# Performance work log

Hardware: AMD Instinct MI355X
Metric: run time of the kernel (lower is better)

## Reference

```python
import jax, jax.numpy as jnp
import numpy as np

HEADS = 16

def setup_inputs() -> dict:
    key = jax.random.key(0)
    ks = jax.random.split(key, 5)
    B, T, D = 2, 2048, 2048
    s = 0.02
    return {
        "x": jax.random.normal(ks[0], (B, T, D), dtype=jnp.float32),
        "Wq": jax.random.normal(ks[1], (D, D), dtype=jnp.float32) * s,
        "Wk": jax.random.normal(ks[2], (D, D), dtype=jnp.float32) * s,
        "Wv": jax.random.normal(ks[3], (D, D), dtype=jnp.float32) * s,
        "Wo": jax.random.normal(ks[4], (D, D), dtype=jnp.float32) * s,
    }

def reference(x, Wq, Wk, Wv, Wo):
    B, T, _ = x.shape
    H = HEADS
    Dh = Wq.shape[1] // H
    # projections: [B,T,H,Dh]
    q = (x @ Wq).reshape(B, T, H, Dh)
    k = (x @ Wk).reshape(B, T, H, Dh)
    v = (x @ Wv).reshape(B, T, H, Dh)
    # raw scores [B,H,T,T]
    scores = jnp.einsum("bthd,bshd->bhts", q, k)
    # NOTE (faithful to source): mask is multiplicative 0/1 tril (the
    # masked_fill(-inf) in the torch code is not in-place and has no effect),
    # and the scale is sqrt(token_len), not sqrt(head_dim).
    mask = jnp.tril(jnp.ones((T, T), dtype=scores.dtype))
    scores = scores * mask
    attn = jax.nn.softmax(scores / (T ** 0.5), axis=-1)
    out = jnp.einsum("bhts,bshd->bthd", attn, v).reshape(B, T, H * Dh)
    return out @ Wo
```

## Files before the change

### kernel.cpp

```cpp
#include <hip/hip_runtime.h>


typedef __attribute__((ext_vector_type(4))) float  f32x4;
typedef __attribute__((ext_vector_type(8))) short  bf16x8;
typedef __attribute__((ext_vector_type(4))) unsigned short u16x4;

#define AS1 __attribute__((address_space(1)))
#define AS3 __attribute__((address_space(3)))

__device__ __forceinline__ void llds16(const void* g, void* l) {
  __builtin_amdgcn_global_load_lds((const AS1 void*)g, (AS3 void*)l, 16, 0, 0);
}

__device__ __forceinline__ unsigned short f2bf(float f) {
  unsigned int u = __builtin_bit_cast(unsigned int, f);
  u += 0x7fffu + ((u >> 16) & 1u);
  return (unsigned short)(u >> 16);
}

__device__ __forceinline__ float bf2f(unsigned short u) {
  return __builtin_bit_cast(float, (unsigned int)u << 16);
}

__global__ __launch_bounds__(256) void cast_x_kernel(const float* __restrict__ in,
                                                     unsigned short* __restrict__ out) {
  int i = blockIdx.x * 256 + threadIdx.x;
  f32x4 v = ((const f32x4*)in)[i];
  u16x4 o;
  o[0] = f2bf(v[0]); o[1] = f2bf(v[1]); o[2] = f2bf(v[2]); o[3] = f2bf(v[3]);
  ((u16x4*)out)[i] = o;
}

__global__ __launch_bounds__(256) void transpose_w_kernel(const float* __restrict__ W,
                                                          unsigned short* __restrict__ Wt) {
  __shared__ float tile[32][33];
  const int bx = blockIdx.x << 5;
  const int by = blockIdx.y << 5;
  const int tx = threadIdx.x;
  const int ty = threadIdx.y;
#pragma unroll
  for (int r = ty; r < 32; r += 8)
    tile[r][tx] = W[(size_t)(bx + r) * 2048 + by + tx];
  __syncthreads();
#pragma unroll
  for (int r = ty; r < 32; r += 8)
    Wt[(size_t)(by + r) * 2048 + bx + tx] = f2bf(tile[tx][r]);
}

template <int OUT>
__global__ __launch_bounds__(256) void gemm_bt(const unsigned short* __restrict__ A,
                                               const unsigned short* __restrict__ Bt,
                                               void* __restrict__ Cv) {
  __shared__ __align__(16) char smem[16384];
  const int tid  = threadIdx.x;
  const int lane = tid & 63;
  const int w    = tid >> 6;
  const int f    = blockIdx.x;
  const int bn   = ((f & 7) << 1) + ((f >> 3) & 1);
  const int bm   = f >> 4;
  const int wr = w >> 1, wc = w & 1;
  const int q16 = lane >> 4;
  const int l15 = lane & 15;

  f32x4 acc[4][4];
#pragma unroll
  for (int i = 0; i < 4; ++i)
#pragma unroll
    for (int j = 0; j < 4; ++j) acc[i][j] = (f32x4){0.f, 0.f, 0.f, 0.f};

  for (int k0 = 0; k0 < 2048; k0 += 32) {
    __syncthreads();
#pragma unroll
    for (int c = 0; c < 2; ++c) {
      int ch  = (w << 1) + c;
      int row = (ch << 4) + (lane >> 2);
      int colb = ((lane & 3) << 4) ^ (((row >> 1) & 3) << 4);
      const unsigned short* srcA = A + (size_t)((bm << 7) + row) * 2048 + k0 + (colb >> 1);
      llds16(srcA, smem + (ch << 10));
      const unsigned short* srcB = Bt + (size_t)((bn << 7) + row) * 2048 + k0 + (colb >> 1);
      llds16(srcB, smem + 8192 + (ch << 10));
    }
    asm volatile("s_waitcnt vmcnt(0)" ::: "memory");
    __syncthreads();

    bf16x8 af[4], bf[4];
#pragma unroll
    for (int mi = 0; mi < 4; ++mi) {
      int row = (wr << 6) + (mi << 4) + l15;
      af[mi] = *(const bf16x8*)(smem + (row << 6) + ((q16 << 4) ^ (((row >> 1) & 3) << 4)));
    }
#pragma unroll
    for (int ni = 0; ni < 4; ++ni) {
      int row = (wc << 6) + (ni << 4) + l15;
      bf[ni] = *(const bf16x8*)(smem + 8192 + (row << 6) + ((q16 << 4) ^ (((row >> 1) & 3) << 4)));
    }
#pragma unroll
    for (int mi = 0; mi < 4; ++mi)
#pragma unroll
      for (int ni = 0; ni < 4; ++ni)
        acc[mi][ni] = __builtin_amdgcn_mfma_f32_16x16x32_bf16(af[mi], bf[ni], acc[mi][ni], 0, 0, 0);
  }

  const int rb = q16 << 2;
#pragma unroll
  for (int mi = 0; mi < 4; ++mi) {
    int m0 = (bm << 7) + (wr << 6) + (mi << 4) + rb;
#pragma unroll
    for (int ni = 0; ni < 4; ++ni) {
      int n = (bn << 7) + (wc << 6) + (ni << 4) + l15;
      if constexpr (OUT == 0) {
        unsigned short* C = (unsigned short*)Cv;
#pragma unroll
        for (int j = 0; j < 4; ++j)
          C[(size_t)(m0 + j) * 2048 + n] = f2bf(acc[mi][ni][j]);
      } else if constexpr (OUT == 1) {
        u16x4 pk;
#pragma unroll
        for (int j = 0; j < 4; ++j) pk[j] = f2bf(acc[mi][ni][j]);
        int b = m0 >> 11, t = m0 & 2047;
        unsigned short* C = (unsigned short*)Cv;
        *(u16x4*)(C + ((size_t)((b << 4) + (n >> 7)) * 128 + (n & 127)) * 2048 + t) = pk;
      } else {
        float* C = (float*)Cv;
#pragma unroll
        for (int j = 0; j < 4; ++j)
          C[(size_t)(m0 + j) * 2048 + n] = acc[mi][ni][j];
      }
    }
  }
}

__global__ __launch_bounds__(256) void vsuf_kernel(const unsigned short* __restrict__ Vt,
                                                   float* __restrict__ Suf) {
  const int row  = blockIdx.x * 4 + (threadIdx.x >> 6);
  const int lane = threadIdx.x & 63;
  const unsigned short* vp = Vt + (size_t)row * 2048 + (lane << 5);
  float a = 0.f;
#pragma unroll
  for (int c = 0; c < 4; ++c) {
    bf16x8 v = *(const bf16x8*)(vp + (c << 3));
#pragma unroll
    for (int j = 0; j < 8; ++j) a += bf2f((unsigned short)v[j]);
  }
  float I = a;
#pragma unroll
  for (int off = 1; off < 64; off <<= 1) {
    float t = __shfl_down(I, off, 64);
    I += (lane + off < 64) ? t : 0.f;
  }
  Suf[(size_t)lane * 4096 + row] = I;
  if (lane == 0) Suf[(size_t)64 * 4096 + row] = 0.f;
}

__global__ __launch_bounds__(256) void attn_kernel(const unsigned short* __restrict__ Q,
                                                   const unsigned short* __restrict__ K,
                                                   const unsigned short* __restrict__ V,
                                                   const float* __restrict__ Suf,
                                                   unsigned short* __restrict__ O) {
  __shared__ __align__(16) char smem[36864];
  const int tid  = threadIdx.x;
  const int lane = tid & 63;
  const int w    = tid >> 6;
  const int q16  = lane >> 4;
  const int l15  = lane & 15;
  const int f    = blockIdx.x;
  const int bh    = ((f & 7) << 2) + ((f >> 3) & 3);
  const int strip = 31 - (f >> 5);
  const int b  = bh >> 4;
  const float scale = 0.02209708691207961f;
  const size_t qkbase = ((size_t)(b << 11)) * 2048 + ((size_t)(bh & 15) << 7);
  const size_t vbase  = (size_t)bh << 18;
  const int rb = q16 << 2;
  char* Psm = smem + 32768 + (w << 10);

  const int numIter = 2 * strip + 2;
  const int t0 = (strip << 6) + (w << 4);

  auto stage = [&](int s0, int kb, int vb) {
#pragma unroll
    for (int c = 0; c < 2; ++c) {
      int ch = (w << 1) + c;
      int rowK = (ch << 2) + q16;
      int colbK = (l15 << 4) ^ ((rowK & 7) << 4);
      llds16(K + qkbase + (size_t)(s0 + rowK) * 2048 + (colbK >> 1), smem + kb + (ch << 10));
      int rowV = (ch << 4) + (lane >> 2);
      int colbV = ((lane & 3) << 4) ^ (((rowV >> 2) & 3) << 4);
      llds16(V + vbase + (size_t)rowV * 2048 + s0 + (colbV >> 1), smem + vb + (ch << 10));
    }
  };

  bf16x8 qf[4];
  {
    const unsigned short* qp = Q + qkbase + (size_t)(t0 + l15) * 2048 + (q16 << 3);
#pragma unroll
    for (int kk = 0; kk < 4; ++kk) qf[kk] = *(const bf16x8*)(qp + (kk << 5));
  }

  f32x4 oacc[8];
#pragma unroll
  for (int i = 0; i < 8; ++i) oacc[i] = (f32x4){0.f, 0.f, 0.f, 0.f};
  float ell[4] = {0.f, 0.f, 0.f, 0.f};

  stage(0, 0, 16384);
  asm volatile("s_waitcnt vmcnt(0)" ::: "memory");
  __syncthreads();

  int cur = 0;
  for (int it = 0; it < numIter; ++it) {
    const int s0 = it << 5;
    if (it + 1 < numIter)
      stage(s0 + 32, (cur ^ 1) << 13, 16384 + ((cur ^ 1) << 13));

    if (s0 <= t0) {
      const int kb = cur << 13;
      const int vb = 16384 + (cur << 13);

      f32x4 sA = (f32x4){0.f, 0.f, 0.f, 0.f}, sB = (f32x4){0.f, 0.f, 0.f, 0.f};
#pragma unroll
      for (int kk = 0; kk < 4; ++kk) {
        int r0 = l15;
        bf16x8 k0f = *(const bf16x8*)(smem + kb + (r0 << 8) + (((kk << 6) + (q16 << 4)) ^ ((r0 & 7) << 4)));
        sA = __builtin_amdgcn_mfma_f32_16x16x32_bf16(qf[kk], k0f, sA, 0, 0, 0);
        int r1 = 16 + l15;
        bf16x8 k1f = *(const bf16x8*)(smem + kb + (r1 << 8) + (((kk << 6) + (q16 << 4)) ^ ((r1 & 7) << 4)));
        sB = __builtin_amdgcn_mfma_f32_16x16x32_bf16(qf[kk], k1f, sB, 0, 0, 0);
      }

      float pA[4], pB[4];
#pragma unroll
      for (int j = 0; j < 4; ++j) {
        int t  = t0 + rb + j;
        int sa = s0 + l15;
        float vA = (sa <= t)      ? sA[j] * scale : 0.f;
        float vB = (sa + 16 <= t) ? sB[j] * scale : 0.f;
        pA[j] = __expf(vA);
        pB[j] = __expf(vB);
        ell[j] += pA[j] + pB[j];
      }

#pragma unroll
      for (int j = 0; j < 4; ++j) {
        int r   = rb + j;
        int swz = ((r >> 1) & 3) << 4;
        *(unsigned short*)(Psm + (r << 6) + ((l15 << 1) ^ swz))        = f2bf(pA[j]);
        *(unsigned short*)(Psm + (r << 6) + ((32 + (l15 << 1)) ^ swz)) = f2bf(pB[j]);
      }
      asm volatile("s_waitcnt lgkmcnt(0)" ::: "memory");

      bf16x8 pa;
      {
        int r = l15;
        pa = *(const bf16x8*)(Psm + (r << 6) + ((q16 << 4) ^ (((r >> 1) & 3) << 4)));
      }
#pragma unroll
      for (int ni = 0; ni < 8; ++ni) {
        int dr = (ni << 4) + l15;
        bf16x8 vbf = *(const bf16x8*)(smem + vb + (dr << 6) + ((q16 << 4) ^ (((dr >> 2) & 3) << 4)));
        oacc[ni] = __builtin_amdgcn_mfma_f32_16x16x32_bf16(pa, vbf, oacc[ni], 0, 0, 0);
      }
    }

    asm volatile("s_waitcnt vmcnt(0)" ::: "memory");
    __syncthreads();
    cur ^= 1;
  }

  const int send = (t0 & ~31) + 32;
  const float* sp = Suf + (size_t)(send >> 5) * 4096 + ((size_t)bh << 7);
  const float extra = (float)(2048 - send);
#pragma unroll
  for (int ni = 0; ni < 8; ++ni) {
    float sv = sp[(ni << 4) + l15];
#pragma unroll
    for (int j = 0; j < 4; ++j) oacc[ni][j] += sv;
  }

#pragma unroll
  for (int j = 0; j < 4; ++j) {
    float r = ell[j];
    r += __shfl_xor(r, 1, 64);
    r += __shfl_xor(r, 2, 64);
    r += __shfl_xor(r, 4, 64);
    r += __shfl_xor(r, 8, 64);
    float inv = 1.0f / (r + extra);
    int t = t0 + rb + j;
    unsigned short* op = O + qkbase + (size_t)t * 2048;
#pragma unroll
    for (int ni = 0; ni < 8; ++ni)
      op[(ni << 4) + l15] = f2bf(oacc[ni][j] * inv);
  }
}

extern "C" void kernel_launch(void* const* d_in, const int* in_sizes, int n_in,
                              void* d_out, int out_size, void* d_ws, size_t ws_size,
                              hipStream_t stream) {
  (void)in_sizes; (void)n_in; (void)out_size; (void)ws_size;
  const float* x  = (const float*)d_in[0];
  const float* Wq = (const float*)d_in[1];
  const float* Wk = (const float*)d_in[2];
  const float* Wv = (const float*)d_in[3];
  const float* Wo = (const float*)d_in[4];
  float* out = (float*)d_out;

  char* ws = (char*)d_ws;
  unsigned short* Xb  = (unsigned short*)(ws);
  unsigned short* Wqt = (unsigned short*)(ws + 16777216);
  unsigned short* Wkt = (unsigned short*)(ws + 16777216 + 8388608);
  unsigned short* Wvt = (unsigned short*)(ws + 16777216 + 2 * 8388608);
  unsigned short* Wot = (unsigned short*)(ws + 16777216 + 3 * 8388608);
  unsigned short* Qb  = (unsigned short*)(ws + 50331648);
  unsigned short* Kb  = (unsigned short*)(ws + 67108864);
  unsigned short* Vt  = (unsigned short*)(ws + 83886080);
  unsigned short* Ob  = Xb;
  float*          Suf = (float*)Wqt;

  cast_x_kernel<<<8192, 256, 0, stream>>>(x, Xb);
  {
    dim3 tb(32, 8), tg(64, 64);
    transpose_w_kernel<<<tg, tb, 0, stream>>>(Wq, Wqt);
    transpose_w_kernel<<<tg, tb, 0, stream>>>(Wk, Wkt);
    transpose_w_kernel<<<tg, tb, 0, stream>>>(Wv, Wvt);
    transpose_w_kernel<<<tg, tb, 0, stream>>>(Wo, Wot);
  }
  gemm_bt<0><<<512, 256, 0, stream>>>(Xb, Wqt, (void*)Qb);
  gemm_bt<0><<<512, 256, 0, stream>>>(Xb, Wkt, (void*)Kb);
  gemm_bt<1><<<512, 256, 0, stream>>>(Xb, Wvt, (void*)Vt);

  vsuf_kernel<<<1024, 256, 0, stream>>>(Vt, Suf);

  attn_kernel<<<1024, 256, 0, stream>>>(Qb, Kb, Vt, Suf, Ob);

  gemm_bt<2><<<512, 256, 0, stream>>>(Ob, Wot, (void*)out);
}
```

Before: 305.8 us.

## Pipeline GEMM with 4-stage LDS buffering and 128x256 tiles per block

Reworks the bf16 GEMM so each 512-thread block computes a 128x256 tile and prefetches three K-steps ahead into a 4-slot LDS ring using global_load_lds. Counted vmcnt waits let global loads overlap MFMA compute. It also remaps block indices for XCD-aware locality and raises wave priority around the MFMAs. The cost is much more LDS per block (96KB), which limits occupancy, and the grid shrinks to 256 blocks, which may leave some CUs underused.

```diff
diff --git a/kernel.cpp b/kernel.cpp
--- a/kernel.cpp
+++ b/kernel.cpp
@@ -48,58 +48,97 @@
 }
 
 template <int OUT>
-__global__ __launch_bounds__(256) void gemm_bt(const unsigned short* __restrict__ A,
-                                               const unsigned short* __restrict__ Bt,
-                                               void* __restrict__ Cv) {
-  __shared__ __align__(16) char smem[16384];
+__global__ __launch_bounds__(512, 2) void gemm_bt(const unsigned short* __restrict__ A,
+                                                  const unsigned short* __restrict__ Bt,
+                                                  void* __restrict__ Cv) {
+  __shared__ __align__(16) char smem[98304];
   const int tid  = threadIdx.x;
   const int lane = tid & 63;
   const int w    = tid >> 6;
   const int f    = blockIdx.x;
-  const int bn   = ((f & 7) << 1) + ((f >> 3) & 1);
-  const int bm   = f >> 4;
-  const int wr = w >> 1, wc = w & 1;
+  const int xcd  = f & 7;
+  const int g    = f >> 3;
+  const int bm   = ((xcd >> 1) << 3) + (g & 7);
+  const int bn   = ((xcd & 1) << 2) + (g >> 3);
+  const int wr = w >> 2, wc = w & 3;
   const int q16 = lane >> 4;
   const int l15 = lane & 15;
 
+  const int aIdx = (w << 6) + lane;
+  const int aRow = aIdx >> 2, aCph = aIdx & 3;
+  const unsigned short* aSrc = A + (size_t)((bm << 7) + aRow) * 2048
+                                 + ((aCph ^ ((aRow >> 1) & 3)) << 3);
+  const int bRow0 = aIdx >> 2, bCph0 = aIdx & 3;
+  const int bIdx1 = 512 + aIdx;
+  const int bRow1 = bIdx1 >> 2, bCph1 = bIdx1 & 3;
+  const unsigned short* bSrc0 = Bt + (size_t)((bn << 8) + bRow0) * 2048
+                                  + ((bCph0 ^ ((bRow0 >> 1) & 3)) << 3);
+  const unsigned short* bSrc1 = Bt + (size_t)((bn << 8) + bRow1) * 2048
+                                  + ((bCph1 ^ ((bRow1 >> 1) & 3)) << 3);
+
+  const int swx = ((q16 ^ ((l15 >> 1) & 3)) << 4);
+  const int aoff = ((wr << 6) + l15) * 64 + swx;
+  const int boff = 8192 + ((wc << 6) + l15) * 64 + swx;
+
   f32x4 acc[4][4];
 #pragma unroll
   for (int i = 0; i < 4; ++i)
 #pragma unroll
     for (int j = 0; j < 4; ++j) acc[i][j] = (f32x4){0.f, 0.f, 0.f, 0.f};
 
-  for (int k0 = 0; k0 < 2048; k0 += 32) {
-    __syncthreads();
-#pragma unroll
-    for (int c = 0; c < 2; ++c) {
-      int ch  = (w << 1) + c;
-      int row = (ch << 4) + (lane >> 2);
-      int colb = ((lane & 3) << 4) ^ (((row >> 1) & 3) << 4);
-      const unsigned short* srcA = A + (size_t)((bm << 7) + row) * 2048 + k0 + (colb >> 1);
-      llds16(srcA, smem + (ch << 10));
-      const unsigned short* srcB = Bt + (size_t)((bn << 7) + row) * 2048 + k0 + (colb >> 1);
-      llds16(srcB, smem + 8192 + (ch << 10));
-    }
-    asm volatile("s_waitcnt vmcnt(0)" ::: "memory");
-    __syncthreads();
-
+  auto stageT = [&](int t, int slot) {
+    char* sb = smem + slot * 24576 + (w << 10);
+    const size_t ko = (size_t)t << 5;
+    llds16(aSrc + ko, sb);
+    llds16(bSrc0 + ko, sb + 8192);
+    llds16(bSrc1 + ko, sb + 16384);
+  };
+
+  auto computeT = [&](int slot) {
+    const char* base = smem + slot * 24576;
     bf16x8 af[4], bf[4];
 #pragma unroll
-    for (int mi = 0; mi < 4; ++mi) {
-      int row = (wr << 6) + (mi << 4) + l15;
-      af[mi] = *(const bf16x8*)(smem + (row << 6) + ((q16 << 4) ^ (((row >> 1) & 3) << 4)));
-    }
-#pragma unroll
-    for (int ni = 0; ni < 4; ++ni) {
-      int row = (wc << 6) + (ni << 4) + l15;
-      bf[ni] = *(const bf16x8*)(smem + 8192 + (row << 6) + ((q16 << 4) ^ (((row >> 1) & 3) << 4)));
-    }
+    for (int mi = 0; mi < 4; ++mi) af[mi] = *(const bf16x8*)(base + aoff + (mi << 10));
+#pragma unroll
+    for (int ni = 0; ni < 4; ++ni) bf[ni] = *(const bf16x8*)(base + boff + (ni << 10));
+    __builtin_amdgcn_s_setprio(1);
 #pragma unroll
     for (int mi = 0; mi < 4; ++mi)
 #pragma unroll
       for (int ni = 0; ni < 4; ++ni)
         acc[mi][ni] = __builtin_amdgcn_mfma_f32_16x16x32_bf16(af[mi], bf[ni], acc[mi][ni], 0, 0, 0);
-  }
+    __builtin_amdgcn_s_setprio(0);
+  };
+
+  stageT(0, 0); stageT(1, 1); stageT(2, 2);
+
+#pragma unroll 1
+  for (int i = 0; i < 60; i += 4) {
+#pragma unroll
+    for (int u = 0; u < 4; ++u) {
+      stageT(i + u + 3, (u + 3) & 3);
+      asm volatile("s_waitcnt vmcnt(9)" ::: "memory");
+      __builtin_amdgcn_s_barrier();
+      computeT(u);
+      __builtin_amdgcn_s_barrier();
+    }
+  }
+  stageT(63, 3);
+  asm volatile("s_waitcnt vmcnt(9)" ::: "memory");
+  __builtin_amdgcn_s_barrier();
+  computeT(0);
+  __builtin_amdgcn_s_barrier();
+  asm volatile("s_waitcnt vmcnt(6)" ::: "memory");
+  __builtin_amdgcn_s_barrier();
+  computeT(1);
+  __builtin_amdgcn_s_barrier();
+  asm volatile("s_waitcnt vmcnt(3)" ::: "memory");
+  __builtin_amdgcn_s_barrier();
+  computeT(2);
+  __builtin_amdgcn_s_barrier();
+  asm volatile("s_waitcnt vmcnt(0)" ::: "memory");
+  __builtin_amdgcn_s_barrier();
+  computeT(3);
 
   const int rb = q16 << 2;
 #pragma unroll
@@ -107,7 +146,7 @@
     int m0 = (bm << 7) + (wr << 6) + (mi << 4) + rb;
 #pragma unroll
     for (int ni = 0; ni < 4; ++ni) {
-      int n = (bn << 7) + (wc << 6) + (ni << 4) + l15;
+      int n = (bn << 8) + (wc << 6) + (ni << 4) + l15;
       if constexpr (OUT == 0) {
         unsigned short* C = (unsigned short*)Cv;
 #pragma unroll
@@ -322,13 +361,13 @@
     transpose_w_kernel<<<tg, tb, 0, stream>>>(Wv, Wvt);
     transpose_w_kernel<<<tg, tb, 0, stream>>>(Wo, Wot);
   }
-  gemm_bt<0><<<512, 256, 0, stream>>>(Xb, Wqt, (void*)Qb);
-  gemm_bt<0><<<512, 256, 0, stream>>>(Xb, Wkt, (void*)Kb);
-  gemm_bt<1><<<512, 256, 0, stream>>>(Xb, Wvt, (void*)Vt);
+  gemm_bt<0><<<256, 512, 0, stream>>>(Xb, Wqt, (void*)Qb);
+  gemm_bt<0><<<256, 512, 0, stream>>>(Xb, Wkt, (void*)Kb);
+  gemm_bt<1><<<256, 512, 0, stream>>>(Xb, Wvt, (void*)Vt);
 
   vsuf_kernel<<<1024, 256, 0, stream>>>(Vt, Suf);
 
   attn_kernel<<<1024, 256, 0, stream>>>(Qb, Kb, Vt, Suf, Ob);
 
-  gemm_bt<2><<<512, 256, 0, stream>>>(Ob, Wot, (void*)out);
-}
+  gemm_bt<2><<<256, 512, 0, stream>>>(Ob, Wot, (void*)out);
+}
```

New measurement: 273.4 us. -10.6%, faster.
